# Performance work log

Measured on AMD Instinct MI355X. Metric: run time of the kernel, lower is better.

## Reference

```python
import jax, jax.numpy as jnp
import numpy as np

D_MODEL = 1024
NUM_HEADS = 16
D_K = D_MODEL // NUM_HEADS
NEG_INF = -1e9


def setup_inputs() -> dict:
    key = jax.random.key(0)
    ks = jax.random.split(key, 9)
    B, S, D = 4, 2048, D_MODEL
    scale = 1.0 / np.sqrt(D)
    inp = {
        "x": jax.random.normal(ks[0], (B, S, D), dtype=jnp.float32),
        "Wq": jax.random.normal(ks[1], (D, D), dtype=jnp.float32) * scale,
        "bq": jnp.zeros((D,), dtype=jnp.float32),
        "Wk": jax.random.normal(ks[2], (D, D), dtype=jnp.float32) * scale,
        "bk": jnp.zeros((D,), dtype=jnp.float32),
        "Wv": jax.random.normal(ks[3], (D, D), dtype=jnp.float32) * scale,
        "bv": jnp.zeros((D,), dtype=jnp.float32),
        "Wo": jax.random.normal(ks[4], (D, D), dtype=jnp.float32) * scale,
        "bo": jnp.zeros((D,), dtype=jnp.float32),
    }
    return inp


def reference(x, Wq, bq, Wk, bk, Wv, bv, Wo, bo):
    B, S, D = x.shape
    H, dk = NUM_HEADS, D_K
    # padding mask: token is pad if any feature == 0; shape [B,1,1,S] (keys)
    mask = (x == 0).any(axis=-1)[:, None, None, :]

    def split_heads(t):  # [B,S,D] -> [B,H,S,dk]
        return t.reshape(B, S, H, dk).transpose(0, 2, 1, 3)

    q = split_heads(x @ Wq + bq)
    k = split_heads(x @ Wk + bk)
    v = split_heads(x @ Wv + bv)

    scores = jnp.einsum("bhqd,bhkd->bhqk", q, k) / np.sqrt(dk).astype(x.dtype)
    scores = jnp.where(mask, jnp.asarray(NEG_INF, x.dtype), scores)
    weights = jax.nn.softmax(scores, axis=-1)
    context = jnp.einsum("bhqk,bhkd->bhqd", weights, v)
    context = context.transpose(0, 2, 1, 3).reshape(B, S, D)
    return context @ Wo + bo
```

## Files before the change

kernel.cpp:

```cpp
#include <hip/hip_runtime.h>
#include <cstdint>
#include <cstddef>

static constexpr int Bz = 4, S = 2048, Dm = 1024, H = 16, DK = 64;
static constexpr int M = Bz * S;

typedef __attribute__((ext_vector_type(8))) short bf16x8;
typedef __attribute__((ext_vector_type(4))) float f32x4;

__device__ __forceinline__ unsigned short f2b(float f) {
    unsigned u = __float_as_uint(f);
    return (unsigned short)((u + 0x7FFFu + ((u >> 16) & 1u)) >> 16);
}

__device__ __forceinline__ unsigned cvtpk(float lo, float hi) {
    unsigned r;
    asm("v_cvt_pk_bf16_f32 %0, %1, %2" : "=v"(r) : "v"(lo), "v"(hi));
    return r;
}

__device__ __forceinline__ float fexp2(float x) {
#if __has_builtin(__builtin_amdgcn_exp2f)
    return __builtin_amdgcn_exp2f(x);
#else
    float r;
    asm("v_exp_f32 %0, %1" : "=v"(r) : "v"(x));
    return r;
#endif
}

__device__ __forceinline__ void gld_lds16(const void* g, void* l) {
    __builtin_amdgcn_global_load_lds(
        (const __attribute__((address_space(1))) unsigned int*)g,
        (__attribute__((address_space(3))) unsigned int*)l, 16, 0, 0);
}

__global__ __launch_bounds__(256) void k_convx(const float* __restrict__ x,
                                               unsigned short* __restrict__ xb,
                                               unsigned char* __restrict__ mask) {
    const int row = blockIdx.x;
    const int t = threadIdx.x;
    const float4 v = *(const float4*)(x + (size_t)row * Dm + t * 4);
    const bool z = (v.x == 0.f) | (v.y == 0.f) | (v.z == 0.f) | (v.w == 0.f);
    ushort4 o;
    o.x = f2b(v.x); o.y = f2b(v.y); o.z = f2b(v.z); o.w = f2b(v.w);
    *(ushort4*)(xb + (size_t)row * Dm + t * 4) = o;
    __shared__ int zf;
    if (t == 0) zf = 0;
    __syncthreads();
    if (z) zf = 1;
    __syncthreads();
    if (t == 0) mask[row] = (unsigned char)zf;
}

__global__ __launch_bounds__(256) void k_convw(const float* __restrict__ Wq, const float* __restrict__ Wk,
                                               const float* __restrict__ Wv, const float* __restrict__ Wo,
                                               unsigned short* __restrict__ Wt) {
    const float* W = (blockIdx.z == 0) ? Wq : (blockIdx.z == 1) ? Wk : (blockIdx.z == 2) ? Wv : Wo;
    unsigned short* o = Wt + (size_t)blockIdx.z * Dm * Dm;
    __shared__ float tile[32][33];
    const int k0 = blockIdx.x * 32, n0 = blockIdx.y * 32;
    const int tx = threadIdx.x, ty = threadIdx.y;
#pragma unroll
    for (int i = 0; i < 4; i++)
        tile[ty + 8 * i][tx] = W[(size_t)(k0 + ty + 8 * i) * Dm + n0 + tx];
    __syncthreads();
#pragma unroll
    for (int i = 0; i < 4; i++)
        o[(size_t)(n0 + ty + 8 * i) * Dm + k0 + tx] = f2b(tile[tx][ty + 8 * i]);
}

template <int MODE>
__global__ __launch_bounds__(256) void k_gemm(
    const unsigned short* __restrict__ A,
    const unsigned short* __restrict__ Bw,
    const float* __restrict__ bias0, const float* __restrict__ bias1, const float* __restrict__ bias2,
    unsigned short* __restrict__ Qo, unsigned short* __restrict__ Ko,
    unsigned short* __restrict__ Vto, float* __restrict__ Co)
{
    __shared__ unsigned short sA[128 * 32];
    __shared__ unsigned short sB[128 * 32];
    const int m0 = blockIdx.x * 128;
    const int gn0 = blockIdx.y * 128;
    const int tid = threadIdx.x;
    const int lane = tid & 63;
    const int wid = tid >> 6;
    const int wm = wid & 1, wn = wid >> 1;
    const int srow = tid >> 2;
    const int sc8 = (tid & 3) * 8;
    const int lr = lane & 15;
    const int lg = lane >> 4;
    f32x4 acc[4][4] = {};
    const unsigned short* Ag = A + (size_t)(m0 + srow) * Dm + sc8;
    const unsigned short* Bg = Bw + (size_t)(gn0 + srow) * Dm + sc8;
    unsigned short* const lA = sA + wid * 512;
    unsigned short* const lB = sB + wid * 512;
    for (int k0 = 0; k0 < Dm; k0 += 32) {
        __syncthreads();
        gld_lds16(Ag + k0, lA);
        gld_lds16(Ag + (size_t)64 * Dm + k0, lA + 2048);
        gld_lds16(Bg + k0, lB);
        gld_lds16(Bg + (size_t)64 * Dm + k0, lB + 2048);
        __syncthreads();
        bf16x8 af[4], bg[4];
#pragma unroll
        for (int mi = 0; mi < 4; mi++)
            af[mi] = *(const bf16x8*)&sA[(wm * 64 + mi * 16 + lr) * 32 + lg * 8];
#pragma unroll
        for (int ni = 0; ni < 4; ni++)
            bg[ni] = *(const bf16x8*)&sB[(wn * 64 + ni * 16 + lr) * 32 + lg * 8];
#pragma unroll
        for (int mi = 0; mi < 4; mi++)
#pragma unroll
            for (int ni = 0; ni < 4; ni++)
                acc[mi][ni] = __builtin_amdgcn_mfma_f32_16x16x32_bf16(af[mi], bg[ni], acc[mi][ni], 0, 0, 0);
    }
#pragma unroll
    for (int mi = 0; mi < 4; mi++) {
        const int row0 = m0 + wm * 64 + mi * 16 + lg * 4;
#pragma unroll
        for (int ni = 0; ni < 4; ni++) {
            const int gn = gn0 + wn * 64 + ni * 16 + lr;
            const int t = gn >> 10;
            const int n = gn & 1023;
            const int h = n >> 6, d = n & 63;
            const float bsv = (MODE == 0)
                ? ((t == 0) ? bias0[n] : (t == 1) ? bias1[n] : bias2[n])
                : bias0[gn];
#pragma unroll
            for (int r = 0; r < 4; r++) {
                const int row = row0 + r;
                const float v = acc[mi][ni][r] + bsv;
                if (MODE == 0) {
                    const int bb = row >> 11;
                    const int s = row & (S - 1);
                    const size_t bh = (size_t)bb * H + h;
                    if (t == 0) {
                        Qo[(bh * S + s) * DK + d] = f2b(v * 0.18033688011f);
                    } else if (t == 1) {
                        Ko[(bh * S + s) * DK + d] = f2b(v);
                    } else {
                        const int k5 = s & 31;
                        const int sp = (s & ~31) | ((k5 & 12) << 1) | ((k5 >> 4) << 2) | (k5 & 3);
                        Vto[(bh * DK + d) * S + sp] = f2b(v);
                    }
                } else {
                    Co[(size_t)row * Dm + gn] = v;
                }
            }
        }
    }
}

__global__ __launch_bounds__(256, 2) void k_attn(
    const unsigned short* __restrict__ Q, const unsigned short* __restrict__ K,
    const unsigned short* __restrict__ Vt, const unsigned char* __restrict__ mask,
    unsigned short* __restrict__ ctx)
{
    __shared__ unsigned short sK[2 * 4096];
    __shared__ unsigned short sV[2 * 4096];
    const int wg = blockIdx.x;
    const int sz = (wg & 7) * 128 + (wg >> 3);
    const int xt = sz & 15;
    const int bh = sz >> 4;
    const int bidx = bh >> 4, h = bh & 15;
    const int tid = threadIdx.x, lane = tid & 63, wid = tid >> 6;
    const int lr = lane & 15, lg = lane >> 4;
    const int qbase = xt * 128 + wid * 32;
    const size_t hoff = (size_t)bh * S * DK;
    const unsigned char* mrow = mask + bidx * S;
    const uint4 mza = *(const uint4*)(mrow + lane * 32);
    const uint4 mzb = *(const uint4*)(mrow + lane * 32 + 16);
    const bool anymask =
        __ballot((mza.x | mza.y | mza.z | mza.w | mzb.x | mzb.y | mzb.z | mzb.w) != 0) != 0ull;
    const unsigned short* qp = Q + hoff + (size_t)(qbase + lr) * DK;
    const bf16x8 aqA0 = *(const bf16x8*)(qp + lg * 8);
    const bf16x8 aqA1 = *(const bf16x8*)(qp + 32 + lg * 8);
    const bf16x8 aqB0 = *(const bf16x8*)(qp + 16 * DK + lg * 8);
    const bf16x8 aqB1 = *(const bf16x8*)(qp + 16 * DK + 32 + lg * 8);
    f32x4 oA[4] = {}, oB[4] = {};
    f32x4 lvA = {}, lvB = {};
    const int rw = lane >> 3;
    const int row0 = wid * 16 + rw;
    const int csrc = ((lane & 7) ^ rw) << 4;
    const char* gK0 = (const char*)(K + hoff) + (size_t)row0 * 128 + csrc;
    const char* gK1 = gK0 + 8 * 128;
    const char* gV0 = (const char*)(Vt + hoff) + (size_t)row0 * (S * 2) + csrc;
    const char* gV1 = gV0 + (size_t)8 * (S * 2);
    constexpr int NT = S / 64;
    unsigned short* const wK = sK + wid * 1024;
    unsigned short* const wV = sV + wid * 1024;

    gld_lds16(gK0, wK);        gld_lds16(gK1, wK + 512);
    gld_lds16(gV0, wV);        gld_lds16(gV1, wV + 512);
    gK0 += 8192; gK1 += 8192; gV0 += 128; gV1 += 128;

    auto body = [&](int t, const char* sKc, const char* sVc, int nbuf) {
        asm volatile("s_waitcnt vmcnt(0)" ::: "memory");
        __builtin_amdgcn_s_barrier();
        __builtin_amdgcn_sched_barrier(0);
        if (t + 1 < NT) {
            gld_lds16(gK0, wK + nbuf * 4096);  gld_lds16(gK1, wK + nbuf * 4096 + 512);
            gld_lds16(gV0, wV + nbuf * 4096);  gld_lds16(gV1, wV + nbuf * 4096 + 512);
            gK0 += 8192; gK1 += 8192; gV0 += 128; gV1 += 128;
        }
        f32x4 zA[4], zB[4];
        __builtin_amdgcn_s_setprio(1);
#pragma unroll
        for (int nt = 0; nt < 4; nt++) {
            const int row = nt * 16 + lr;
            const int sw = (row & 7) << 4;
            const bf16x8 kf0 = *(const bf16x8*)(sKc + ((row * 128 + lg * 16) ^ sw));
            const bf16x8 kf1 = *(const bf16x8*)(sKc + ((row * 128 + 64 + lg * 16) ^ sw));
            f32x4 a = {};
            a = __builtin_amdgcn_mfma_f32_16x16x32_bf16(kf0, aqA0, a, 0, 0, 0);
            zA[nt] = __builtin_amdgcn_mfma_f32_16x16x32_bf16(kf1, aqA1, a, 0, 0, 0);
            f32x4 b = {};
            b = __builtin_amdgcn_mfma_f32_16x16x32_bf16(kf0, aqB0, b, 0, 0, 0);
            zB[nt] = __builtin_amdgcn_mfma_f32_16x16x32_bf16(kf1, aqB1, b, 0, 0, 0);
        }
        __builtin_amdgcn_s_setprio(0);
        if (anymask) {
            const unsigned long long bal = __ballot(mrow[t * 64 + lane] != 0);
            if (bal) {
#pragma unroll
                for (int nt = 0; nt < 4; nt++)
#pragma unroll
                    for (int r = 0; r < 4; r++)
                        if ((bal >> (nt * 16 + lg * 4 + r)) & 1) { zA[nt][r] = -1e9f; zB[nt][r] = -1e9f; }
            }
        }
        union { unsigned u[4]; bf16x8 v; } wA0, wA1, wB0, wB1;
#pragma unroll
        for (int nt = 0; nt < 4; nt++) {
#pragma unroll
            for (int r = 0; r < 4; r++) zA[nt][r] = fexp2(zA[nt][r]);
            lvA += zA[nt];
        }
        wA0.u[0] = cvtpk(zA[0][0], zA[0][1]); wA0.u[1] = cvtpk(zA[0][2], zA[0][3]);
        wA0.u[2] = cvtpk(zA[1][0], zA[1][1]); wA0.u[3] = cvtpk(zA[1][2], zA[1][3]);
        wA1.u[0] = cvtpk(zA[2][0], zA[2][1]); wA1.u[1] = cvtpk(zA[2][2], zA[2][3]);
        wA1.u[2] = cvtpk(zA[3][0], zA[3][1]); wA1.u[3] = cvtpk(zA[3][2], zA[3][3]);
#pragma unroll
        for (int nt = 0; nt < 4; nt++) {
#pragma unroll
            for (int r = 0; r < 4; r++) zB[nt][r] = fexp2(zB[nt][r]);
            lvB += zB[nt];
        }
        wB0.u[0] = cvtpk(zB[0][0], zB[0][1]); wB0.u[1] = cvtpk(zB[0][2], zB[0][3]);
        wB0.u[2] = cvtpk(zB[1][0], zB[1][1]); wB0.u[3] = cvtpk(zB[1][2], zB[1][3]);
        wB1.u[0] = cvtpk(zB[2][0], zB[2][1]); wB1.u[1] = cvtpk(zB[2][2], zB[2][3]);
        wB1.u[2] = cvtpk(zB[3][0], zB[3][1]); wB1.u[3] = cvtpk(zB[3][2], zB[3][3]);
        __builtin_amdgcn_s_setprio(1);
#pragma unroll
        for (int dt = 0; dt < 4; dt++) {
            const int row = dt * 16 + lr;
            const int sw = (row & 7) << 4;
            const bf16x8 v0 = *(const bf16x8*)(sVc + ((row * 128 + lg * 16) ^ sw));
            const bf16x8 v1 = *(const bf16x8*)(sVc + ((row * 128 + 64 + lg * 16) ^ sw));
            oA[dt] = __builtin_amdgcn_mfma_f32_16x16x32_bf16(wA0.v, v0, oA[dt], 0, 0, 0);
            oA[dt] = __builtin_amdgcn_mfma_f32_16x16x32_bf16(wA1.v, v1, oA[dt], 0, 0, 0);
            oB[dt] = __builtin_amdgcn_mfma_f32_16x16x32_bf16(wB0.v, v0, oB[dt], 0, 0, 0);
            oB[dt] = __builtin_amdgcn_mfma_f32_16x16x32_bf16(wB1.v, v1, oB[dt], 0, 0, 0);
        }
        __builtin_amdgcn_s_setprio(0);
        asm volatile("s_waitcnt lgkmcnt(0)" ::: "memory");
    };

    const char* const sKb0 = (const char*)sK;
    const char* const sKb1 = sKb0 + 8192;
    const char* const sVb0 = (const char*)sV;
    const char* const sVb1 = sVb0 + 8192;
    for (int t = 0; t < NT; t += 2) {
        body(t,     sKb0, sVb0, 1);
        body(t + 1, sKb1, sVb1, 0);
    }

    float lsA = (lvA[0] + lvA[1]) + (lvA[2] + lvA[3]);
    lsA += __shfl_xor(lsA, 16, 64);
    lsA += __shfl_xor(lsA, 32, 64);
    float lsB = (lvB[0] + lvB[1]) + (lvB[2] + lvB[3]);
    lsB += __shfl_xor(lsB, 16, 64);
    lsB += __shfl_xor(lsB, 32, 64);
#pragma unroll
    for (int r = 0; r < 4; r++) {
        const float iA = 1.f / __shfl(lsA, lg * 4 + r, 16);
        const float iB = 1.f / __shfl(lsB, lg * 4 + r, 16);
        const int sA_ = qbase + lg * 4 + r;
#pragma unroll
        for (int dt = 0; dt < 4; dt++) {
            const int col = h * 64 + dt * 16 + lr;
            ctx[((size_t)bidx * S + sA_) * Dm + col]      = f2b(oA[dt][r] * iA);
            ctx[((size_t)bidx * S + sA_ + 16) * Dm + col] = f2b(oB[dt][r] * iB);
        }
    }
}

extern "C" void kernel_launch(void* const* d_in, const int* in_sizes, int n_in,
                              void* d_out, int out_size, void* d_ws, size_t ws_size,
                              hipStream_t stream)
{
    (void)in_sizes; (void)n_in; (void)out_size; (void)ws_size;
    const float* x  = (const float*)d_in[0];
    const float* Wq = (const float*)d_in[1];
    const float* bq = (const float*)d_in[2];
    const float* Wk = (const float*)d_in[3];
    const float* bk = (const float*)d_in[4];
    const float* Wv = (const float*)d_in[5];
    const float* bv = (const float*)d_in[6];
    const float* Wo = (const float*)d_in[7];
    const float* bo = (const float*)d_in[8];
    float* out = (float*)d_out;
    char* ws = (char*)d_ws;
    unsigned short* xb  = (unsigned short*)(ws);
    unsigned short* Wt  = (unsigned short*)(ws + ((size_t)16 << 20));
    unsigned short* Qb  = (unsigned short*)(ws + ((size_t)24 << 20));
    unsigned short* Kb  = (unsigned short*)(ws + ((size_t)40 << 20));
    unsigned short* Vtb = (unsigned short*)(ws + ((size_t)56 << 20));
    unsigned short* ctx = (unsigned short*)(ws + ((size_t)72 << 20));
    unsigned char*  msk = (unsigned char*)(ws + ((size_t)88 << 20));

    k_convx<<<dim3(M), dim3(256), 0, stream>>>(x, xb, msk);
    k_convw<<<dim3(Dm / 32, Dm / 32, 4), dim3(32, 8), 0, stream>>>(Wq, Wk, Wv, Wo, Wt);
    k_gemm<0><<<dim3(M / 128, 3072 / 128), dim3(256), 0, stream>>>(
        xb, Wt, bq, bk, bv, Qb, Kb, Vtb, nullptr);
    k_attn<<<dim3(Bz * H * (S / 128)), dim3(256), 0, stream>>>(Qb, Kb, Vtb, msk, ctx);
    k_gemm<1><<<dim3(M / 128, 1024 / 128), dim3(256), 0, stream>>>(
        ctx, Wt + (size_t)3 * Dm * Dm, bo, nullptr, nullptr, nullptr, nullptr, nullptr, out);
}
```

Measured before the change: 201.2 us.

## Halve attention KV tile to 32 keys and merge conversion kernels

The attention kernel now streams K/V in 32-key tiles instead of 64. This halves LDS usage and per-iteration register pressure but doubles the number of barrier-synchronized iterations, and it adds a new V swizzle layout. Separately, the x conversion and the weight transpose/convert kernels are merged into one launch to save a kernel launch. Smaller tiles mean less MFMA work per barrier and more sync overhead.

```diff
diff --git a/kernel.cpp b/kernel.cpp
--- a/kernel.cpp
+++ b/kernel.cpp
@@ -35,39 +35,44 @@
         (__attribute__((address_space(3))) unsigned int*)l, 16, 0, 0);
 }
 
-__global__ __launch_bounds__(256) void k_convx(const float* __restrict__ x,
-                                               unsigned short* __restrict__ xb,
-                                               unsigned char* __restrict__ mask) {
-    const int row = blockIdx.x;
-    const int t = threadIdx.x;
-    const float4 v = *(const float4*)(x + (size_t)row * Dm + t * 4);
-    const bool z = (v.x == 0.f) | (v.y == 0.f) | (v.z == 0.f) | (v.w == 0.f);
-    ushort4 o;
-    o.x = f2b(v.x); o.y = f2b(v.y); o.z = f2b(v.z); o.w = f2b(v.w);
-    *(ushort4*)(xb + (size_t)row * Dm + t * 4) = o;
-    __shared__ int zf;
-    if (t == 0) zf = 0;
-    __syncthreads();
-    if (z) zf = 1;
-    __syncthreads();
-    if (t == 0) mask[row] = (unsigned char)zf;
-}
-
-__global__ __launch_bounds__(256) void k_convw(const float* __restrict__ Wq, const float* __restrict__ Wk,
-                                               const float* __restrict__ Wv, const float* __restrict__ Wo,
-                                               unsigned short* __restrict__ Wt) {
-    const float* W = (blockIdx.z == 0) ? Wq : (blockIdx.z == 1) ? Wk : (blockIdx.z == 2) ? Wv : Wo;
-    unsigned short* o = Wt + (size_t)blockIdx.z * Dm * Dm;
-    __shared__ float tile[32][33];
-    const int k0 = blockIdx.x * 32, n0 = blockIdx.y * 32;
-    const int tx = threadIdx.x, ty = threadIdx.y;
-#pragma unroll
-    for (int i = 0; i < 4; i++)
-        tile[ty + 8 * i][tx] = W[(size_t)(k0 + ty + 8 * i) * Dm + n0 + tx];
-    __syncthreads();
-#pragma unroll
-    for (int i = 0; i < 4; i++)
-        o[(size_t)(n0 + ty + 8 * i) * Dm + k0 + tx] = f2b(tile[tx][ty + 8 * i]);
+__global__ __launch_bounds__(256) void k_conv(const float* __restrict__ x,
+                                              const float* __restrict__ Wq, const float* __restrict__ Wk,
+                                              const float* __restrict__ Wv, const float* __restrict__ Wo,
+                                              unsigned short* __restrict__ xb,
+                                              unsigned char* __restrict__ mask,
+                                              unsigned short* __restrict__ Wt) {
+    const int bid = blockIdx.x;
+    const int tid = threadIdx.x;
+    if (bid < M) {
+        const int row = bid;
+        const float4 v = *(const float4*)(x + (size_t)row * Dm + tid * 4);
+        const bool z = (v.x == 0.f) | (v.y == 0.f) | (v.z == 0.f) | (v.w == 0.f);
+        ushort4 o;
+        o.x = f2b(v.x); o.y = f2b(v.y); o.z = f2b(v.z); o.w = f2b(v.w);
+        *(ushort4*)(xb + (size_t)row * Dm + tid * 4) = o;
+        __shared__ int zf;
+        if (tid == 0) zf = 0;
+        __syncthreads();
+        if (z) zf = 1;
+        __syncthreads();
+        if (tid == 0) mask[row] = (unsigned char)zf;
+    } else {
+        const int wb = bid - M;
+        const int zidx = wb >> 10;
+        const int rem = wb & 1023;
+        const int k0 = (rem & 31) * 32, n0 = (rem >> 5) * 32;
+        const float* W = (zidx == 0) ? Wq : (zidx == 1) ? Wk : (zidx == 2) ? Wv : Wo;
+        unsigned short* o = Wt + (size_t)zidx * Dm * Dm;
+        __shared__ float tile[32][33];
+        const int tx = tid & 31, ty = tid >> 5;
+#pragma unroll
+        for (int i = 0; i < 4; i++)
+            tile[ty + 8 * i][tx] = W[(size_t)(k0 + ty + 8 * i) * Dm + n0 + tx];
+        __syncthreads();
+#pragma unroll
+        for (int i = 0; i < 4; i++)
+            o[(size_t)(n0 + ty + 8 * i) * Dm + k0 + tx] = f2b(tile[tx][ty + 8 * i]);
+    }
 }
 
 template <int MODE>
@@ -157,8 +162,8 @@
     const unsigned short* __restrict__ Vt, const unsigned char* __restrict__ mask,
     unsigned short* __restrict__ ctx)
 {
-    __shared__ unsigned short sK[2 * 4096];
-    __shared__ unsigned short sV[2 * 4096];
+    __shared__ unsigned short sK[2 * 2048];
+    __shared__ unsigned short sV[2 * 2048];
     const int wg = blockIdx.x;
     const int sz = (wg & 7) * 128 + (wg >> 3);
     const int xt = sz & 15;
@@ -180,34 +185,33 @@
     const bf16x8 aqB1 = *(const bf16x8*)(qp + 16 * DK + 32 + lg * 8);
     f32x4 oA[4] = {}, oB[4] = {};
     f32x4 lvA = {}, lvB = {};
-    const int rw = lane >> 3;
-    const int row0 = wid * 16 + rw;
-    const int csrc = ((lane & 7) ^ rw) << 4;
-    const char* gK0 = (const char*)(K + hoff) + (size_t)row0 * 128 + csrc;
-    const char* gK1 = gK0 + 8 * 128;
-    const char* gV0 = (const char*)(Vt + hoff) + (size_t)row0 * (S * 2) + csrc;
-    const char* gV1 = gV0 + (size_t)8 * (S * 2);
-    constexpr int NT = S / 64;
-    unsigned short* const wK = sK + wid * 1024;
-    unsigned short* const wV = sV + wid * 1024;
-
-    gld_lds16(gK0, wK);        gld_lds16(gK1, wK + 512);
-    gld_lds16(gV0, wV);        gld_lds16(gV1, wV + 512);
-    gK0 += 8192; gK1 += 8192; gV0 += 128; gV1 += 128;
+    const int rwk = lane >> 3;
+    const int csK = ((lane & 7) ^ rwk) << 4;
+    const char* gK = (const char*)(K + hoff) + (size_t)(wid * 8 + rwk) * 128 + csK;
+    const int rv = lane >> 2;
+    const int csV = ((lane & 3) ^ ((rv >> 1) & 3)) << 4;
+    const char* gV = (const char*)(Vt + hoff) + (size_t)(wid * 16 + rv) * (S * 2) + csV;
+    constexpr int NT = S / 32;
+    unsigned short* const wKd = sK + wid * 512;
+    unsigned short* const wVd = sV + wid * 512;
+
+    gld_lds16(gK, wKd);
+    gld_lds16(gV, wVd);
+    gK += 4096; gV += 64;
 
     auto body = [&](int t, const char* sKc, const char* sVc, int nbuf) {
         asm volatile("s_waitcnt vmcnt(0)" ::: "memory");
         __builtin_amdgcn_s_barrier();
         __builtin_amdgcn_sched_barrier(0);
         if (t + 1 < NT) {
-            gld_lds16(gK0, wK + nbuf * 4096);  gld_lds16(gK1, wK + nbuf * 4096 + 512);
-            gld_lds16(gV0, wV + nbuf * 4096);  gld_lds16(gV1, wV + nbuf * 4096 + 512);
-            gK0 += 8192; gK1 += 8192; gV0 += 128; gV1 += 128;
-        }
-        f32x4 zA[4], zB[4];
+            gld_lds16(gK, wKd + nbuf * 2048);
+            gld_lds16(gV, wVd + nbuf * 2048);
+            gK += 4096; gV += 64;
+        }
+        f32x4 zA[2], zB[2];
         __builtin_amdgcn_s_setprio(1);
 #pragma unroll
-        for (int nt = 0; nt < 4; nt++) {
+        for (int nt = 0; nt < 2; nt++) {
             const int row = nt * 16 + lr;
             const int sw = (row & 7) << 4;
             const bf16x8 kf0 = *(const bf16x8*)(sKc + ((row * 128 + lg * 16) ^ sw));
@@ -221,56 +225,50 @@
         }
         __builtin_amdgcn_s_setprio(0);
         if (anymask) {
-            const unsigned long long bal = __ballot(mrow[t * 64 + lane] != 0);
+            const unsigned long long bal =
+                __ballot(mrow[t * 32 + (lane & 31)] != 0) & 0xFFFFFFFFull;
             if (bal) {
 #pragma unroll
-                for (int nt = 0; nt < 4; nt++)
+                for (int nt = 0; nt < 2; nt++)
 #pragma unroll
                     for (int r = 0; r < 4; r++)
                         if ((bal >> (nt * 16 + lg * 4 + r)) & 1) { zA[nt][r] = -1e9f; zB[nt][r] = -1e9f; }
             }
         }
-        union { unsigned u[4]; bf16x8 v; } wA0, wA1, wB0, wB1;
-#pragma unroll
-        for (int nt = 0; nt < 4; nt++) {
+        union { unsigned u[4]; bf16x8 v; } wA0, wB0;
+#pragma unroll
+        for (int nt = 0; nt < 2; nt++) {
 #pragma unroll
             for (int r = 0; r < 4; r++) zA[nt][r] = fexp2(zA[nt][r]);
             lvA += zA[nt];
         }
         wA0.u[0] = cvtpk(zA[0][0], zA[0][1]); wA0.u[1] = cvtpk(zA[0][2], zA[0][3]);
         wA0.u[2] = cvtpk(zA[1][0], zA[1][1]); wA0.u[3] = cvtpk(zA[1][2], zA[1][3]);
-        wA1.u[0] = cvtpk(zA[2][0], zA[2][1]); wA1.u[1] = cvtpk(zA[2][2], zA[2][3]);
-        wA1.u[2] = cvtpk(zA[3][0], zA[3][1]); wA1.u[3] = cvtpk(zA[3][2], zA[3][3]);
-#pragma unroll
-        for (int nt = 0; nt < 4; nt++) {
+#pragma unroll
+        for (int nt = 0; nt < 2; nt++) {
 #pragma unroll
             for (int r = 0; r < 4; r++) zB[nt][r] = fexp2(zB[nt][r]);
             lvB += zB[nt];
         }
         wB0.u[0] = cvtpk(zB[0][0], zB[0][1]); wB0.u[1] = cvtpk(zB[0][2], zB[0][3]);
         wB0.u[2] = cvtpk(zB[1][0], zB[1][1]); wB0.u[3] = cvtpk(zB[1][2], zB[1][3]);
-        wB1.u[0] = cvtpk(zB[2][0], zB[2][1]); wB1.u[1] = cvtpk(zB[2][2], zB[2][3]);
-        wB1.u[2] = cvtpk(zB[3][0], zB[3][1]); wB1.u[3] = cvtpk(zB[3][2], zB[3][3]);
         __builtin_amdgcn_s_setprio(1);
 #pragma unroll
         for (int dt = 0; dt < 4; dt++) {
             const int row = dt * 16 + lr;
-            const int sw = (row & 7) << 4;
-            const bf16x8 v0 = *(const bf16x8*)(sVc + ((row * 128 + lg * 16) ^ sw));
-            const bf16x8 v1 = *(const bf16x8*)(sVc + ((row * 128 + 64 + lg * 16) ^ sw));
+            const int sw = (row >> 1) & 3;
+            const bf16x8 v0 = *(const bf16x8*)(sVc + row * 64 + ((lg ^ sw) << 4));
             oA[dt] = __builtin_amdgcn_mfma_f32_16x16x32_bf16(wA0.v, v0, oA[dt], 0, 0, 0);
-            oA[dt] = __builtin_amdgcn_mfma_f32_16x16x32_bf16(wA1.v, v1, oA[dt], 0, 0, 0);
             oB[dt] = __builtin_amdgcn_mfma_f32_16x16x32_bf16(wB0.v, v0, oB[dt], 0, 0, 0);
-            oB[dt] = __builtin_amdgcn_mfma_f32_16x16x32_bf16(wB1.v, v1, oB[dt], 0, 0, 0);
         }
         __builtin_amdgcn_s_setprio(0);
         asm volatile("s_waitcnt lgkmcnt(0)" ::: "memory");
     };
 
     const char* const sKb0 = (const char*)sK;
-    const char* const sKb1 = sKb0 + 8192;
+    const char* const sKb1 = sKb0 + 4096;
     const char* const sVb0 = (const char*)sV;
-    const char* const sVb1 = sVb0 + 8192;
+    const char* const sVb1 = sVb0 + 4096;
     for (int t = 0; t < NT; t += 2) {
         body(t,     sKb0, sVb0, 1);
         body(t + 1, sKb1, sVb1, 0);
@@ -320,8 +318,7 @@
     unsigned short* ctx = (unsigned short*)(ws + ((size_t)72 << 20));
     unsigned char*  msk = (unsigned char*)(ws + ((size_t)88 << 20));
 
-    k_convx<<<dim3(M), dim3(256), 0, stream>>>(x, xb, msk);
-    k_convw<<<dim3(Dm / 32, Dm / 32, 4), dim3(32, 8), 0, stream>>>(Wq, Wk, Wv, Wo, Wt);
+    k_conv<<<dim3(M + 4096), dim3(256), 0, stream>>>(x, Wq, Wk, Wv, Wo, xb, msk, Wt);
     k_gemm<0><<<dim3(M / 128, 3072 / 128), dim3(256), 0, stream>>>(
         xb, Wt, bq, bk, bv, Qb, Kb, Vtb, nullptr);
     k_attn<<<dim3(Bz * H * (S / 128)), dim3(256), 0, stream>>>(Qb, Kb, Vtb, msk, ctx);
```

New measurement: 196.7 us, median of 2. 2.2% less time.
